# Kernel optimization log

Hardware: AMD Instinct MI355X
Metric: run time of the kernel (lower is better)

## Reference

```python
import jax, jax.numpy as jnp
import numpy as np

B, S, D_MODEL, N_HEAD = 8, 512, 1024, 16
HEAD_DIM = D_MODEL // N_HEAD


def _pos_embed(seq_len, dim):
    # RelativeSinusoidalPositionalEmbedding(dim, padding_idx=0, init_size=1200)
    num = 1201  # init_size + 1
    half = dim // 2
    freq = np.exp(np.arange(half, dtype=np.float32) * (-np.log(10000.0) / (half - 1)))
    pos = np.arange(-((num + 1) // 2), num // 2, dtype=np.float32)  # tf.range(-num//2, num//2), python floor div
    emb = pos[:, None] * freq[None, :]
    table = np.concatenate([np.sin(emb), np.cos(emb)], axis=1).astype(np.float32)  # [num, dim]
    table[0] = 0.0  # padding_idx = 0
    origin_shift = num // 2 + 1  # 601
    idx = np.arange(-seq_len, seq_len) + origin_shift
    return jnp.asarray(table[idx])  # [2*seq_len, dim]


def setup_inputs() -> dict:
    key = jax.random.key(0)
    k1, k2, k3, k4 = jax.random.split(key, 4)
    return {
        "x": jax.random.normal(k1, (B, S, D_MODEL), dtype=jnp.float32),
        "mask": jnp.ones((B, S), dtype=jnp.int32),
        "Wqv": jax.random.normal(k2, (D_MODEL, 2 * D_MODEL), dtype=jnp.float32) * 0.02,
        "r_r_bias": jax.random.normal(k3, (N_HEAD, HEAD_DIM), dtype=jnp.float32) * 0.02,
        "r_w_bias": jax.random.normal(k4, (N_HEAD, HEAD_DIM), dtype=jnp.float32) * 0.02,
    }


def _shift(BD):
    # [b, h, s, 2s] -> [b, h, s, s] via pad-reshape trick
    b, h, s, _ = BD.shape
    zp = jnp.zeros((b, h, s, 1), BD.dtype)
    BD = jnp.concatenate([BD, zp], axis=-1).reshape(b, h, 2 * s + 1, s)
    BD = BD[:, :, :-1].reshape(b, h, s, 2 * s)
    return BD[:, :, :, s:]


def reference(x, mask, Wqv, r_r_bias, r_w_bias):
    pos = _pos_embed(S, HEAD_DIM)  # [2S, head_dim], stop-gradient constant
    qv = x @ Wqv  # [B, S, 2*D]
    q, v = jnp.split(qv, 2, axis=-1)

    def heads(t):
        return t.reshape(B, S, N_HEAD, HEAD_DIM).transpose(0, 2, 1, 3)  # bhsd

    q, k, v = heads(q), heads(x), heads(v)
    rw_q = q + r_r_bias[None, :, None, :]
    AC = jnp.einsum('bhqd,bhkd->bhqk', rw_q, k)
    D_ = jnp.einsum('hd,ld->hl', r_w_bias, pos)[None, :, None, :]  # [1, h, 1, 2S]
    B_ = jnp.einsum('bhqd,ld->bhql', q, pos)  # [b, h, S, 2S]
    BD = _shift(B_ + D_)
    attn = AC + BD  # scale=False -> divide by 1
    m = mask.astype(jnp.float32)[:, None, None, :]
    attn = attn * m - (1.0 - m) * 1e8
    attn = jax.nn.softmax(attn, axis=-1)  # dropout is identity at inference
    out = jnp.einsum('bhqk,bhkd->bhqd', attn, v)
    return out.transpose(0, 2, 1, 3).reshape(B, S, D_MODEL)
```

## Files before the change

### kernel.cpp

```cpp
#include <hip/hip_runtime.h>


using h4 = __attribute__((ext_vector_type(4))) _Float16;
using h8 = __attribute__((ext_vector_type(8))) _Float16;
using f32x4 = __attribute__((ext_vector_type(4))) float;

#define MFMA16(a, b, c) __builtin_amdgcn_mfma_f32_16x16x32_f16((a), (b), (c), 0, 0, 0)

#define GLOAD_LDS16(gp, lp)                                                        \
  __builtin_amdgcn_global_load_lds(                                                \
      (const __attribute__((address_space(1))) unsigned int*)(gp),                 \
      (__attribute__((address_space(3))) unsigned int*)(lp), 16, 0, 0)

__global__ __launch_bounds__(256) void k_prep(const float* __restrict__ x,
                                              const float* __restrict__ Wqv,
                                              _Float16* __restrict__ xh,
                                              _Float16* __restrict__ wT,
                                              _Float16* __restrict__ posP) {
  __shared__ _Float16 t[64][72];
  int bid = blockIdx.x;
  int tid = threadIdx.x;
  if (bid < 2048) {
    size_t idx = (size_t)bid * 256 + tid;
    const float* src = x + idx * 8;
    _Float16 tmp[8];
#pragma unroll
    for (int j = 0; j < 8; ++j) tmp[j] = (_Float16)src[j];
    *(h8*)(xh + idx * 8) = *(const h8*)tmp;
  } else if (bid < 2176) {
    int idx = (bid - 2048) * 256 + tid;
    int tt = idx >> 6, j = idx & 63;
    int jj = j & 31;
    float f = expf((float)jj * (-9.210340371976184f / 31.0f));
    float ang = (float)tt * f;
    posP[idx] = (_Float16)((j < 32) ? sinf(ang) : cosf(ang));
  } else {
    int b2 = bid - 2176;
    int bk = b2 & 15, bn = b2 >> 4;
    int k0 = bk * 64, n0 = bn * 64;
    int r = tid >> 2, c = (tid & 3) * 16;
    const float* src = Wqv + (size_t)(k0 + r) * 2048 + n0 + c;
#pragma unroll
    for (int j = 0; j < 16; ++j) t[r][c + j] = (_Float16)src[j];
    __syncthreads();
    _Float16 tmp[16];
#pragma unroll
    for (int j = 0; j < 16; ++j) tmp[j] = t[c + j][r];
    _Float16* dst = wT + (size_t)(n0 + r) * 1024 + k0 + c;
    *(h8*)dst = *(const h8*)tmp;
    *(h8*)(dst + 8) = *(const h8*)(tmp + 8);
  }
}

__global__ __launch_bounds__(256) void k_gemm(const _Float16* __restrict__ xh,
                                              const _Float16* __restrict__ wT,
                                              const float* __restrict__ rr,
                                              const float* __restrict__ rw,
                                              _Float16* __restrict__ qrr,
                                              _Float16* __restrict__ qrwp,
                                              _Float16* __restrict__ vT) {
  __shared__ _Float16 At[2][128 * 32];
  __shared__ _Float16 Bt[2][128 * 32];

  int bid = blockIdx.x;
  int bm = bid & 31, bn = bid >> 5;
  int tid = threadIdx.x;
  int w = tid >> 6, lane = tid & 63;
  int lr = lane & 15, lg = lane >> 4;

  const _Float16* gA = xh + (size_t)(bm * 128 + 32 * w + (lane >> 2)) * 1024 + (lane & 3) * 8;
  const _Float16* gB = wT + (size_t)(bn * 128 + 32 * w + (lane >> 2)) * 1024 + (lane & 3) * 8;

  auto stage = [&](int bufi, int k0) {
    GLOAD_LDS16(gA + k0, &At[bufi][(32 * w) * 32]);
    GLOAD_LDS16(gA + 16 * 1024 + k0, &At[bufi][(32 * w + 16) * 32]);
    GLOAD_LDS16(gB + k0, &Bt[bufi][(32 * w) * 32]);
    GLOAD_LDS16(gB + 16 * 1024 + k0, &Bt[bufi][(32 * w + 16) * 32]);
  };

  int wm = w >> 1, wn = w & 1;
  f32x4 acc[4][4] = {};

  stage(0, 0);
  __syncthreads();
  int buf = 0;
  for (int i = 0; i < 32; ++i) {
    if (i < 31) stage(buf ^ 1, (i + 1) * 32);
    const _Float16* la = &At[buf][(wm * 64 + lr) * 32 + lg * 8];
    const _Float16* lb = &Bt[buf][(wn * 64 + lr) * 32 + lg * 8];
    h8 af[4], bf[4];
#pragma unroll
    for (int mi = 0; mi < 4; ++mi) af[mi] = *(const h8*)(la + mi * 512);
#pragma unroll
    for (int ni = 0; ni < 4; ++ni) bf[ni] = *(const h8*)(lb + ni * 512);
#pragma unroll
    for (int mi = 0; mi < 4; ++mi)
#pragma unroll
      for (int ni = 0; ni < 4; ++ni)
        acc[mi][ni] = MFMA16(af[mi], bf[ni], acc[mi][ni]);
    __syncthreads();
    buf ^= 1;
  }

  int hg = bn * 2 + wn;
  int mb = bm * 128 + wm * 64;
  if (hg < 16) {
    int h = hg;
    float rrv[4], rwv[4];
#pragma unroll
    for (int ni = 0; ni < 4; ++ni) {
      rrv[ni] = rr[h * 64 + ni * 16 + lr];
      rwv[ni] = rw[h * 64 + ni * 16 + lr];
    }
    float f0 = expf((float)lr * (-9.210340371976184f / 31.0f));
    float f1 = expf((float)(16 + lr) * (-9.210340371976184f / 31.0f));
#pragma unroll
    for (int mi = 0; mi < 4; ++mi)
#pragma unroll
      for (int r = 0; r < 4; ++r) {
        int m = mb + mi * 16 + lg * 4 + r;
        int b = m >> 9, s = m & 511;
        size_t base = ((size_t)(b * 16 + h) * 512 + s) * 64;
#pragma unroll
        for (int ni = 0; ni < 4; ++ni)
          qrr[base + ni * 16 + lr] = (_Float16)(acc[mi][ni][r] + rrv[ni]);
        {
          float qs = acc[mi][0][r] + rwv[0], qc = acc[mi][2][r] + rwv[2];
          float sn, cs;
          sincosf((float)s * f0, &sn, &cs);
          qrwp[base + lr] = (_Float16)(qs * cs + qc * sn);
          qrwp[base + lr + 32] = (_Float16)(qc * cs - qs * sn);
        }
        {
          float qs = acc[mi][1][r] + rwv[1], qc = acc[mi][3][r] + rwv[3];
          float sn, cs;
          sincosf((float)s * f1, &sn, &cs);
          qrwp[base + 16 + lr] = (_Float16)(qs * cs + qc * sn);
          qrwp[base + 16 + lr + 32] = (_Float16)(qc * cs - qs * sn);
        }
      }
  } else {
    int h = hg - 16;
#pragma unroll
    for (int mi = 0; mi < 4; ++mi) {
      int m = mb + mi * 16 + lg * 4;
      int b = m >> 9, s0 = m & 511;
      size_t vtbase = (size_t)(b * 16 + h) * 64 * 512;
#pragma unroll
      for (int ni = 0; ni < 4; ++ni) {
        int d = ni * 16 + lr;
        _Float16 t4[4];
#pragma unroll
        for (int r = 0; r < 4; ++r) t4[r] = (_Float16)acc[mi][ni][r];
        *(h4*)(vT + vtbase + (size_t)d * 512 + s0) = *(const h4*)t4;
      }
    }
  }
}

__global__ __launch_bounds__(256, 2) void k_attn(const _Float16* __restrict__ xh,
                                                 const _Float16* __restrict__ qrr,
                                                 const _Float16* __restrict__ qrwp,
                                                 const _Float16* __restrict__ vT,
                                                 const _Float16* __restrict__ posPg,
                                                 const int* __restrict__ mask,
                                                 float* __restrict__ out) {
  __shared__ _Float16 Kp[128 * 128];
  __shared__ _Float16 Vt[64 * 128];
  __shared__ _Float16 Pl[4][16 * 136];
  __shared__ float Ma[512];

  int bid = blockIdx.x;
  int qb = bid >> 7, h = bid & 15, b = (bid >> 4) & 7;
  int q0 = qb * 128;
  int tid = threadIdx.x;
  int w = tid >> 6, lane = tid & 63;
  int lr = lane & 15, lg = lane >> 4;

  const size_t bh = (size_t)(b * 16 + h);
  const _Float16* kb = xh + (size_t)b * 512 * 1024 + h * 64;
  const _Float16* vTp = vT + bh * 64 * 512;
  const int* mrow = mask + b * 512;

  auto stage = [&](int t0s) {
#pragma unroll
    for (int it = 0; it < 8; ++it) {
      int a = w * 512 + it * 64 + lane;
      int trow = a >> 4, c16 = a & 15;
      int c16s = c16 ^ (trow & 15);
      const _Float16* g = (c16s < 8)
          ? kb + (size_t)(t0s + trow) * 1024 + c16s * 8
          : posPg + (size_t)(t0s + trow) * 64 + (c16s - 8) * 8;
      GLOAD_LDS16(g, &Kp[(size_t)(w * 512 + it * 64) * 8]);
    }
#pragma unroll
    for (int it = 0; it < 4; ++it) {
      int a = w * 256 + it * 64 + lane;
      int drow = a >> 4, c16 = a & 15;
      int c16s = c16 ^ (drow & 15);
      const _Float16* g = vTp + (size_t)drow * 512 + t0s + c16s * 8;
      GLOAD_LDS16(g, &Vt[(size_t)(w * 256 + it * 64) * 8]);
    }
  };

  Ma[tid] = (1.f - (float)mrow[tid]) * -1e8f;
  Ma[tid + 256] = (1.f - (float)mrow[tid + 256]) * -1e8f;

  h8 ar0[2], ar1[2], aw0[2], aw1[2];
#pragma unroll
  for (int rg = 0; rg < 2; ++rg) {
    const _Float16* qrr_p = qrr + (bh * 512 + q0 + 32 * w + 16 * rg + lr) * 64 + lg * 8;
    const _Float16* qrw_p = qrwp + (bh * 512 + q0 + 32 * w + 16 * rg + lr) * 64 + lg * 8;
    ar0[rg] = *(const h8*)(qrr_p);
    ar1[rg] = *(const h8*)(qrr_p + 32);
    aw0[rg] = *(const h8*)(qrw_p);
    aw1[rg] = *(const h8*)(qrw_p + 32);
  }

  float m_run[2][4], l_run[2][4];
  f32x4 O[2][4];
#pragma unroll
  for (int rg = 0; rg < 2; ++rg)
#pragma unroll
    for (int r = 0; r < 4; ++r) {
      m_run[rg][r] = -1e30f;
      l_run[rg][r] = 0.f;
      O[rg][r] = (f32x4){0.f, 0.f, 0.f, 0.f};
    }

  _Float16* pw = &Pl[w][0];

  for (int t0 = 0; t0 < 512; t0 += 128) {
    stage(t0);
    __syncthreads();

#pragma unroll
    for (int rg = 0; rg < 2; ++rg) {
      float s[8][4];
#pragma unroll
      for (int tf = 0; tf < 8; ++tf) {
        int row = tf * 16 + lr;
        const _Float16* bp = &Kp[row * 128];
        h8 b0 = *(const h8*)(bp + ((0 + lg) ^ lr) * 8);
        h8 b1 = *(const h8*)(bp + ((4 + lg) ^ lr) * 8);
        h8 b2 = *(const h8*)(bp + ((8 + lg) ^ lr) * 8);
        h8 b3 = *(const h8*)(bp + ((12 + lg) ^ lr) * 8);
        f32x4 c = {0.f, 0.f, 0.f, 0.f};
        c = MFMA16(ar0[rg], b0, c);
        c = MFMA16(ar1[rg], b1, c);
        c = MFMA16(aw0[rg], b2, c);
        c = MFMA16(aw1[rg], b3, c);
        float ma = Ma[t0 + tf * 16 + lr];
#pragma unroll
        for (int r = 0; r < 4; ++r) s[tf][r] = c[r] + ma;
      }

#pragma unroll
      for (int r = 0; r < 4; ++r) {
        float rm = s[0][r];
#pragma unroll
        for (int tf = 1; tf < 8; ++tf) rm = fmaxf(rm, s[tf][r]);
#pragma unroll
        for (int d = 1; d < 16; d <<= 1) rm = fmaxf(rm, __shfl_xor(rm, d));
        float mn = fmaxf(m_run[rg][r], rm);
        float sc = __expf(m_run[rg][r] - mn);
        m_run[rg][r] = mn;
        float rs = 0.f;
#pragma unroll
        for (int tf = 0; tf < 8; ++tf) {
          float p = __expf(s[tf][r] - mn);
          _Float16 p16 = (_Float16)p;
          pw[(lg * 4 + r) * 136 + tf * 16 + lr] = p16;
          rs += (float)p16;
        }
#pragma unroll
        for (int d = 1; d < 16; d <<= 1) rs += __shfl_xor(rs, d);
        l_run[rg][r] = l_run[rg][r] * sc + rs;
#pragma unroll
        for (int df = 0; df < 4; ++df) O[rg][df][r] *= sc;
      }

      h8 pa[4];
#pragma unroll
      for (int ks = 0; ks < 4; ++ks)
        pa[ks] = *(const h8*)(pw + lr * 136 + ks * 32 + lg * 8);
#pragma unroll
      for (int df = 0; df < 4; ++df) {
        int row = df * 16 + lr;
        const _Float16* vbp = &Vt[row * 128];
#pragma unroll
        for (int ks = 0; ks < 4; ++ks) {
          h8 vb = *(const h8*)(vbp + ((ks * 4 + lg) ^ lr) * 8);
          O[rg][df] = MFMA16(pa[ks], vb, O[rg][df]);
        }
      }
    }
    __syncthreads();
  }

#pragma unroll
  for (int rg = 0; rg < 2; ++rg)
#pragma unroll
    for (int df = 0; df < 4; ++df)
#pragma unroll
      for (int r = 0; r < 4; ++r) {
        int ii = 32 * w + 16 * rg + lg * 4 + r;
        out[((size_t)b * 512 + q0 + ii) * 1024 + h * 64 + df * 16 + lr] =
            O[rg][df][r] / l_run[rg][r];
      }
}

extern "C" void kernel_launch(void* const* d_in, const int* in_sizes, int n_in,
                              void* d_out, int out_size, void* d_ws, size_t ws_size,
                              hipStream_t stream) {
  const float* x = (const float*)d_in[0];
  const int* mask = (const int*)d_in[1];
  const float* Wqv = (const float*)d_in[2];
  const float* rr = (const float*)d_in[3];
  const float* rw = (const float*)d_in[4];
  float* out = (float*)d_out;
  char* ws = (char*)d_ws;
  const size_t MB = 1024 * 1024;
  _Float16* xh = (_Float16*)(ws);
  _Float16* wT = (_Float16*)(ws + 8 * MB);
  _Float16* posP = (_Float16*)(ws + 12 * MB);
  _Float16* qrr = (_Float16*)(ws + 13 * MB);
  _Float16* qrwp = (_Float16*)(ws + 21 * MB);
  _Float16* vT = (_Float16*)(ws + 29 * MB);

  k_prep<<<2688, 256, 0, stream>>>(x, Wqv, xh, wT, posP);
  k_gemm<<<512, 256, 0, stream>>>(xh, wT, rr, rw, qrr, qrwp, vT);
  k_attn<<<512, 256, 0, stream>>>(xh, qrr, qrwp, vT, posP, mask, out);
}
```

Measured before the change: 78.73 us.

## Widen GEMM K-tile with swizzled LDS, use exp2 softmax and MFMA priority hints

```diff
diff --git a/kernel.cpp b/kernel.cpp
--- a/kernel.cpp
+++ b/kernel.cpp
@@ -11,6 +11,8 @@
   __builtin_amdgcn_global_load_lds(                                                \
       (const __attribute__((address_space(1))) unsigned int*)(gp),                 \
       (__attribute__((address_space(3))) unsigned int*)(lp), 16, 0, 0)
+
+#define L2E 1.4426950408889634f
 
 __global__ __launch_bounds__(256) void k_prep(const float* __restrict__ x,
                                               const float* __restrict__ Wqv,
@@ -59,8 +61,8 @@
                                               _Float16* __restrict__ qrr,
                                               _Float16* __restrict__ qrwp,
                                               _Float16* __restrict__ vT) {
-  __shared__ _Float16 At[2][128 * 32];
-  __shared__ _Float16 Bt[2][128 * 32];
+  __shared__ _Float16 At[2][128 * 64];
+  __shared__ _Float16 Bt[2][128 * 64];
 
   int bid = blockIdx.x;
   int bm = bid & 31, bn = bid >> 5;
@@ -68,14 +70,21 @@
   int w = tid >> 6, lane = tid & 63;
   int lr = lane & 15, lg = lane >> 4;
 
-  const _Float16* gA = xh + (size_t)(bm * 128 + 32 * w + (lane >> 2)) * 1024 + (lane & 3) * 8;
-  const _Float16* gB = wT + (size_t)(bn * 128 + 32 * w + (lane >> 2)) * 1024 + (lane & 3) * 8;
-
   auto stage = [&](int bufi, int k0) {
-    GLOAD_LDS16(gA + k0, &At[bufi][(32 * w) * 32]);
-    GLOAD_LDS16(gA + 16 * 1024 + k0, &At[bufi][(32 * w + 16) * 32]);
-    GLOAD_LDS16(gB + k0, &Bt[bufi][(32 * w) * 32]);
-    GLOAD_LDS16(gB + 16 * 1024 + k0, &Bt[bufi][(32 * w + 16) * 32]);
+#pragma unroll
+    for (int it = 0; it < 4; ++it) {
+      int a = w * 256 + it * 64 + lane;
+      int trow = a >> 3, c8s = (a & 7) ^ (trow & 7);
+      GLOAD_LDS16(xh + (size_t)(bm * 128 + trow) * 1024 + k0 + c8s * 8,
+                  &At[bufi][a * 8]);
+    }
+#pragma unroll
+    for (int it = 0; it < 4; ++it) {
+      int a = w * 256 + it * 64 + lane;
+      int trow = a >> 3, c8s = (a & 7) ^ (trow & 7);
+      GLOAD_LDS16(wT + (size_t)(bn * 128 + trow) * 1024 + k0 + c8s * 8,
+                  &Bt[bufi][a * 8]);
+    }
   };
 
   int wm = w >> 1, wn = w & 1;
@@ -84,20 +93,27 @@
   stage(0, 0);
   __syncthreads();
   int buf = 0;
-  for (int i = 0; i < 32; ++i) {
-    if (i < 31) stage(buf ^ 1, (i + 1) * 32);
-    const _Float16* la = &At[buf][(wm * 64 + lr) * 32 + lg * 8];
-    const _Float16* lb = &Bt[buf][(wn * 64 + lr) * 32 + lg * 8];
-    h8 af[4], bf[4];
-#pragma unroll
-    for (int mi = 0; mi < 4; ++mi) af[mi] = *(const h8*)(la + mi * 512);
-#pragma unroll
-    for (int ni = 0; ni < 4; ++ni) bf[ni] = *(const h8*)(lb + ni * 512);
-#pragma unroll
-    for (int mi = 0; mi < 4; ++mi)
-#pragma unroll
-      for (int ni = 0; ni < 4; ++ni)
-        acc[mi][ni] = MFMA16(af[mi], bf[ni], acc[mi][ni]);
+  for (int i = 0; i < 16; ++i) {
+    if (i < 15) stage(buf ^ 1, (i + 1) * 64);
+#pragma unroll
+    for (int kk = 0; kk < 2; ++kk) {
+      h8 af[4], bf[4];
+#pragma unroll
+      for (int mi = 0; mi < 4; ++mi) {
+        int row = wm * 64 + mi * 16 + lr;
+        af[mi] = *(const h8*)(&At[buf][row * 64 + (((kk * 4 + lg) ^ (lr & 7)) * 8)]);
+      }
+#pragma unroll
+      for (int ni = 0; ni < 4; ++ni) {
+        int row = wn * 64 + ni * 16 + lr;
+        bf[ni] = *(const h8*)(&Bt[buf][row * 64 + (((kk * 4 + lg) ^ (lr & 7)) * 8)]);
+      }
+#pragma unroll
+      for (int mi = 0; mi < 4; ++mi)
+#pragma unroll
+        for (int ni = 0; ni < 4; ++ni)
+          acc[mi][ni] = MFMA16(af[mi], bf[ni], acc[mi][ni]);
+    }
     __syncthreads();
     buf ^= 1;
   }
@@ -123,20 +139,20 @@
         size_t base = ((size_t)(b * 16 + h) * 512 + s) * 64;
 #pragma unroll
         for (int ni = 0; ni < 4; ++ni)
-          qrr[base + ni * 16 + lr] = (_Float16)(acc[mi][ni][r] + rrv[ni]);
+          qrr[base + ni * 16 + lr] = (_Float16)((acc[mi][ni][r] + rrv[ni]) * L2E);
         {
           float qs = acc[mi][0][r] + rwv[0], qc = acc[mi][2][r] + rwv[2];
           float sn, cs;
-          sincosf((float)s * f0, &sn, &cs);
-          qrwp[base + lr] = (_Float16)(qs * cs + qc * sn);
-          qrwp[base + lr + 32] = (_Float16)(qc * cs - qs * sn);
+          __sincosf((float)s * f0, &sn, &cs);
+          qrwp[base + lr] = (_Float16)((qs * cs + qc * sn) * L2E);
+          qrwp[base + lr + 32] = (_Float16)((qc * cs - qs * sn) * L2E);
         }
         {
           float qs = acc[mi][1][r] + rwv[1], qc = acc[mi][3][r] + rwv[3];
           float sn, cs;
-          sincosf((float)s * f1, &sn, &cs);
-          qrwp[base + 16 + lr] = (_Float16)(qs * cs + qc * sn);
-          qrwp[base + 16 + lr + 32] = (_Float16)(qc * cs - qs * sn);
+          __sincosf((float)s * f1, &sn, &cs);
+          qrwp[base + 16 + lr] = (_Float16)((qs * cs + qc * sn) * L2E);
+          qrwp[base + 16 + lr + 32] = (_Float16)((qc * cs - qs * sn) * L2E);
         }
       }
   } else {
@@ -203,8 +219,8 @@
     }
   };
 
-  Ma[tid] = (1.f - (float)mrow[tid]) * -1e8f;
-  Ma[tid + 256] = (1.f - (float)mrow[tid + 256]) * -1e8f;
+  Ma[tid] = (1.f - (float)mrow[tid]) * -1.4426950e8f;
+  Ma[tid + 256] = (1.f - (float)mrow[tid + 256]) * -1.4426950e8f;
 
   h8 ar0[2], ar1[2], aw0[2], aw1[2];
 #pragma unroll
@@ -237,6 +253,7 @@
 #pragma unroll
     for (int rg = 0; rg < 2; ++rg) {
       float s[8][4];
+      __builtin_amdgcn_s_setprio(1);
 #pragma unroll
       for (int tf = 0; tf < 8; ++tf) {
         int row = tf * 16 + lr;
@@ -254,6 +271,7 @@
 #pragma unroll
         for (int r = 0; r < 4; ++r) s[tf][r] = c[r] + ma;
       }
+      __builtin_amdgcn_s_setprio(0);
 
 #pragma unroll
       for (int r = 0; r < 4; ++r) {
@@ -263,12 +281,12 @@
 #pragma unroll
         for (int d = 1; d < 16; d <<= 1) rm = fmaxf(rm, __shfl_xor(rm, d));
         float mn = fmaxf(m_run[rg][r], rm);
-        float sc = __expf(m_run[rg][r] - mn);
+        float sc = exp2f(m_run[rg][r] - mn);
         m_run[rg][r] = mn;
         float rs = 0.f;
 #pragma unroll
         for (int tf = 0; tf < 8; ++tf) {
-          float p = __expf(s[tf][r] - mn);
+          float p = exp2f(s[tf][r] - mn);
           _Float16 p16 = (_Float16)p;
           pw[(lg * 4 + r) * 136 + tf * 16 + lr] = p16;
           rs += (float)p16;
@@ -284,6 +302,7 @@
 #pragma unroll
       for (int ks = 0; ks < 4; ++ks)
         pa[ks] = *(const h8*)(pw + lr * 136 + ks * 32 + lg * 8);
+      __builtin_amdgcn_s_setprio(1);
 #pragma unroll
       for (int df = 0; df < 4; ++df) {
         int row = df * 16 + lr;
@@ -294,6 +313,7 @@
           O[rg][df] = MFMA16(pa[ks], vb, O[rg][df]);
         }
       }
+      __builtin_amdgcn_s_setprio(0);
     }
     __syncthreads();
   }
```

Result: faster. 72.23 us (-8.3%).
